# Kernel optimization log

Hardware: AMD Instinct MI355X
Metric: run time of the kernel (lower is better)

## Reference

```python
import jax, jax.numpy as jnp
import numpy as np

B, T, DM, DS = 8, 2048, 1024, 256
BASE_DECAY = 0.05


def _lin(k, out_dim, in_dim):
    return jax.random.normal(k, (out_dim, in_dim), jnp.float32) / np.sqrt(in_dim).astype(np.float32)


def setup_inputs() -> dict:
    key = jax.random.key(0)
    ks = jax.random.split(key, 18)
    return {
        "x": jax.random.normal(ks[0], (B, T, DM), jnp.float32),
        "prev_state": jax.random.normal(ks[1], (B, DS), jnp.float32),
        "W_in": _lin(ks[2], DS, DM),
        "W_x": _lin(ks[3], DS, DM),
        "W_s": _lin(ks[4], DS, DS),
        "W_out": _lin(ks[5], DM, DS),
        "W_gx": _lin(ks[6], DS, DM),
        "b_gx": jax.random.normal(ks[7], (DS,), jnp.float32) * 0.02,
        "W_gs": _lin(ks[8], DS, DS),
        "b_gs": jax.random.normal(ks[9], (DS,), jnp.float32) * 0.02,
        "W_dc": _lin(ks[10], DS, DM + DS),
        "b_dc": jax.random.normal(ks[11], (DS,), jnp.float32) * 0.02,
        "W_pp": _lin(ks[12], DS, 2 * DS),
        "b_pp": jax.random.normal(ks[13], (DS,), jnp.float32) * 0.02,
        "W_pg": _lin(ks[14], DS, DS),
        "b_pg": jax.random.normal(ks[15], (DS,), jnp.float32) * 0.02,
    }


def reference(x, prev_state, W_in, W_x, W_s, W_out, W_gx, b_gx, W_gs, b_gs,
              W_dc, b_dc, W_pp, b_pp, W_pg, b_pg):
    # torch Linear: y = x @ W.T (+ b); W is [out, in]
    lin = lambda v, W: jnp.einsum('bti,oi->bto', v, W)
    Bx, Tx, _ = x.shape
    delta = lin(x, W_in)                                   # [B,T,DS]
    s_prev = jnp.broadcast_to(prev_state[:, None, :], (Bx, Tx, prev_state.shape[-1]))
    ctx = jnp.concatenate([x, s_prev], axis=-1)            # [B,T,DM+DS]
    decay = jnp.exp(-BASE_DECAY * jnp.clip(jax.nn.sigmoid(lin(ctx, W_dc) + b_dc), 0.0, 1.0))
    s_pred = s_prev * decay + delta + lin(x, W_x) + 0.5 * lin(s_prev, W_s)
    perturb_in = jnp.concatenate([s_pred, s_prev], axis=-1)  # [B,T,2*DS]
    perturb_vec = jnp.tanh(lin(perturb_in, W_pp) + b_pp)
    perturb_strength = jax.nn.sigmoid(lin(s_prev, W_pg) + b_pg)
    s_corrected = s_pred + perturb_strength * perturb_vec
    gate_in = jax.nn.sigmoid(lin(x, W_gx) + b_gx)
    gate_state = jax.nn.sigmoid(lin(s_prev, W_gs) + b_gs)
    h = s_corrected * gate_in * gate_state
    out = lin(h, W_out)                                    # [B,T,DM]
    return out, h[:, -1, :]
```

## Files before the change

kernel.cpp:

```cpp
#include <hip/hip_runtime.h>
#include <hip/hip_bf16.h>
#include <math.h>


typedef __attribute__((ext_vector_type(4)))  float f32x4;
typedef __attribute__((ext_vector_type(8)))  short bf16x8;

#define DEV static __device__ __forceinline__

DEV float bf2f(short u) {
  union { float f; unsigned i; } v; v.i = ((unsigned)(unsigned short)u) << 16; return v.f;
}
DEV short f2bf(float f) {
  union { float f; unsigned i; } v; v.f = f;
  unsigned x = v.i;
  return (short)((x + 0x7fffu + ((x >> 16) & 1u)) >> 16);
}
DEV unsigned pk_bf16(float lo, float hi) {
  __hip_bfloat162 h = __float22bfloat162_rn(make_float2(lo, hi));
  return *(unsigned*)&h;
}
DEV float sigmoidf_(float x) { return 1.f / (1.f + expf(-x)); }

DEV void gl16(const void* g, void* l) {
  __builtin_amdgcn_global_load_lds(
      (const __attribute__((address_space(1))) void*)(g),
      (__attribute__((address_space(3))) void*)(l), 16, 0, 0);
}

static const size_t OFF_Y    = 0;
static const size_t OFF_XBF  = 25165824;
static const size_t OFF_S    = OFF_XBF;
static const size_t OFF_G    = OFF_XBF + 8388608;
static const size_t OFF_WCAT = OFF_XBF + 33554432;
static const size_t OFF_WPP  = OFF_WCAT + 1572864;
static const size_t OFF_WOUT = OFF_WPP + 131072;
static const size_t OFF_VEC  = OFF_WOUT + 524288;

__global__ __launch_bounds__(256, 1) void prep_all_k(
    const float* __restrict__ x, short* __restrict__ xbf,
    const float* __restrict__ W_in, const float* __restrict__ W_x,
    const float* __restrict__ W_gx, const float* __restrict__ W_dc,
    const float* __restrict__ W_pp, const float* __restrict__ W_out,
    short* __restrict__ wcat, short* __restrict__ wpp, short* __restrict__ wout,
    const float* __restrict__ prev, const float* __restrict__ Ws,
    const float* __restrict__ bdc, const float* __restrict__ bpp,
    const float* __restrict__ Wpg, const float* __restrict__ bpg,
    const float* __restrict__ Wgs, const float* __restrict__ bgs,
    float* __restrict__ vecs) {
  const int bid = (int)blockIdx.x, tid = (int)threadIdx.x;
  if (bid < 8192) {
    const size_t i = ((size_t)bid * 256 + tid) * 8;
    const float4 a = *(const float4*)(x + i);
    const float4 b = *(const float4*)(x + i + 4);
    uint4 o;
    o.x = pk_bf16(a.x, a.y); o.y = pk_bf16(a.z, a.w);
    o.z = pk_bf16(b.x, b.y); o.w = pk_bf16(b.z, b.w);
    *(uint4*)(xbf + i) = o;
  } else if (bid < 12544) {
    const int idx = (bid - 8192) * 256 + tid;
    const int N_WCAT = 768 * 1024, N_WPP = 256 * 256;
    if (idx < N_WCAT) {
      const int r = idx >> 10, k = idx & 1023;
      float v;
      if (r < 256)      v = W_in[r * 1024 + k] + W_x[r * 1024 + k];
      else if (r < 512) v = W_gx[(r - 256) * 1024 + k];
      else              v = W_dc[(r - 512) * 1280 + k];
      wcat[idx] = f2bf(v);
    } else if (idx < N_WCAT + N_WPP) {
      const int j = idx - N_WCAT, o = j >> 8, k = j & 255;
      wpp[j] = f2bf(W_pp[o * 512 + k]);
    } else {
      const int j = idx - N_WCAT - N_WPP, o = j >> 8, k = j & 255;
      wout[j] = f2bf(W_out[o * 256 + k]);
    }
  } else {
    const int sb = bid - 12544;
    const int b = sb / 20, rem = sb % 20, m = rem >> 2, oq = rem & 3;
    const int lane = tid & 63, w = tid >> 6;
    const float4 sv = *(const float4*)(prev + b * 256 + lane * 4);
    const float* Wb; const float* bias; int stride, off;
    if (m == 0)      { Wb = W_dc; stride = 1280; off = 1024; bias = bdc; }
    else if (m == 1) { Wb = Ws;   stride = 256;  off = 0;    bias = nullptr; }
    else if (m == 2) { Wb = W_pp; stride = 512;  off = 256;  bias = bpp; }
    else if (m == 3) { Wb = Wpg;  stride = 256;  off = 0;    bias = bpg; }
    else             { Wb = Wgs;  stride = 256;  off = 0;    bias = bgs; }
    const int o0 = oq * 64 + w * 16;
#pragma unroll 4
    for (int i = 0; i < 16; ++i) {
      const int o = o0 + i;
      const float4 wv = *(const float4*)(Wb + (size_t)o * stride + off + lane * 4);
      float p = wv.x * sv.x + wv.y * sv.y + wv.z * sv.z + wv.w * sv.w;
#pragma unroll
      for (int d = 32; d >= 1; d >>= 1) p += __shfl_xor(p, d, 64);
      if (lane == 0) {
        float r = (m == 1) ? 0.5f * p : p + bias[o];
        if (m >= 3) r = sigmoidf_(r);
        vecs[m * 2048 + b * 256 + o] = r;
      }
    }
  }
}

__global__ __launch_bounds__(512, 2) void gemm1_8p_k(const short* __restrict__ A,
                                                     const short* __restrict__ Bm,
                                                     short* __restrict__ Y) {
  __shared__ short As[4][8192];
  __shared__ short Bs[4][8192];
  const int tid = (int)threadIdx.x, lane = tid & 63, w = tid >> 6;
  const int wm = w >> 2, wn = w & 3;
  int bid = (int)blockIdx.x;
  bid = (bid & 7) * 24 + (bid >> 3);
  const int mt = bid / 3, nt = bid % 3;
  const int m0 = mt * 256;
  const short* gA = A + (size_t)m0 * 1024;
  const short* gB = Bm + (size_t)(nt * 256) * 1024;

  f32x4 acc[8][4];
#pragma unroll
  for (int mi = 0; mi < 8; ++mi)
#pragma unroll
    for (int ni = 0; ni < 4; ++ni)
#pragma unroll
      for (int r = 0; r < 4; ++r) acc[mi][ni][r] = 0.f;

#define STG(gax, lds, half, t)                                                \
  {                                                                           \
    _Pragma("unroll")                                                         \
    for (int j = 0; j < 2; ++j) {                                             \
      const int G = j * 512 + tid, r = G >> 3, g = G & 7;                     \
      gl16(gax + (size_t)((half) * 128 + r) * 1024 + (t) * 64 +               \
               ((g ^ (r & 7)) * 8),                                           \
           (lds) + G * 8);                                                    \
    }                                                                         \
  }

  STG(gA, As[0], 0, 0); STG(gA, As[1], 1, 0);
  STG(gB, Bs[0], 0, 0); STG(gB, Bs[1], 1, 0);
  STG(gA, As[2], 0, 1);
  asm volatile("s_waitcnt vmcnt(2)" ::: "memory");
  __builtin_amdgcn_s_barrier();

  const int arow = lane & 15, ag = lane >> 4;
  bf16x8 af[4][2], bfv[2][2];
#pragma unroll 1
  for (int t = 0; t < 16; ++t) {
    const short* sA = As[(2 * t + wm) & 3];
    const short* sB = Bs[(2 * t + (wn >> 1)) & 3];
#pragma unroll
    for (int q = 0; q < 4; ++q) {
      const int qm = q >> 1, qn = q & 1;
      if (qn == 0) {
#pragma unroll
        for (int fi = 0; fi < 4; ++fi) {
          const int r = qm * 64 + fi * 16 + arow;
#pragma unroll
          for (int ks = 0; ks < 2; ++ks)
            af[fi][ks] = *(const bf16x8*)(sA + r * 64 + (((ks * 4 + ag) ^ (r & 7)) << 3));
        }
      }
#pragma unroll
      for (int fj = 0; fj < 2; ++fj) {
        const int r = (wn & 1) * 64 + qn * 32 + fj * 16 + arow;
#pragma unroll
        for (int ks = 0; ks < 2; ++ks)
          bfv[fj][ks] = *(const bf16x8*)(sB + r * 64 + (((ks * 4 + ag) ^ (r & 7)) << 3));
      }
      if (q == 0) {
        if (t + 1 < 16) {
          STG(gB, Bs[(2 * t + 2) & 3], 0, t + 1);
          STG(gA, As[(2 * t + 3) & 3], 1, t + 1);
          STG(gB, Bs[(2 * t + 3) & 3], 1, t + 1);
        }
      } else if (q == 3) {
        if (t + 2 < 16) STG(gA, As[(2 * t + 4) & 3], 0, t + 2);
        if (t <= 13)      { asm volatile("s_waitcnt vmcnt(2)" ::: "memory"); }
        else if (t == 14) { asm volatile("s_waitcnt vmcnt(0)" ::: "memory"); }
      }
      __builtin_amdgcn_s_barrier();
      asm volatile("s_waitcnt lgkmcnt(0)" ::: "memory");
      __builtin_amdgcn_sched_barrier(0);
      __builtin_amdgcn_s_setprio(1);
#pragma unroll
      for (int fi = 0; fi < 4; ++fi)
#pragma unroll
        for (int fj = 0; fj < 2; ++fj)
#pragma unroll
          for (int ks = 0; ks < 2; ++ks)
            acc[qm * 4 + fi][qn * 2 + fj] = __builtin_amdgcn_mfma_f32_16x16x32_bf16(
                af[fi][ks], bfv[fj][ks], acc[qm * 4 + fi][qn * 2 + fj], 0, 0, 0);
      __builtin_amdgcn_s_setprio(0);
      __builtin_amdgcn_s_barrier();
    }
  }
#undef STG

#pragma unroll
  for (int mi = 0; mi < 8; ++mi)
#pragma unroll
    for (int ni = 0; ni < 4; ++ni) {
      const int col = nt * 256 + wn * 64 + ni * 16 + (lane & 15);
#pragma unroll
      for (int r = 0; r < 4; ++r) {
        const int row = m0 + wm * 128 + mi * 16 + (lane >> 4) * 4 + r;
        Y[(size_t)row * 768 + col] = f2bf(acc[mi][ni][r]);
      }
    }
}

__global__ __launch_bounds__(256, 1) void elem1_k(const short* __restrict__ Y,
                                                  const float* __restrict__ prev,
                                                  const float* __restrict__ bgx,
                                                  const float* __restrict__ vecs,
                                                  short* __restrict__ S,
                                                  short* __restrict__ G) {
  const int t = (int)blockIdx.x * 256 + (int)threadIdx.x;
  const int row = t >> 5, gi = t & 31, j0 = gi * 8;
  const int b = row >> 11;
  const short* yr = Y + (size_t)row * 768;
  const bf16x8 yix = *(const bf16x8*)(yr + j0);
  const bf16x8 ygx = *(const bf16x8*)(yr + 256 + j0);
  const bf16x8 ydc = *(const bf16x8*)(yr + 512 + j0);
  bf16x8 so, go;
#pragma unroll
  for (int j = 0; j < 8; ++j) {
    const int c = b * 256 + j0 + j;
    const float dcl = bf2f(ydc[j]) + vecs[0 * 2048 + c];
    const float dec = expf(-0.05f * sigmoidf_(dcl));
    const float sp = prev[c] * dec + bf2f(yix[j]) + vecs[1 * 2048 + c];
    const float g = sigmoidf_(bf2f(ygx[j]) + bgx[j0 + j]);
    so[j] = f2bf(sp); go[j] = f2bf(g);
  }
  *(bf16x8*)(S + (size_t)row * 256 + j0) = so;
  *(bf16x8*)(G + (size_t)row * 256 + j0) = go;
}

__global__ __launch_bounds__(256) void gemm2h_k(const short* __restrict__ S,
                                                const short* __restrict__ G,
                                                const short* __restrict__ Wpp,
                                                const float* __restrict__ vecs,
                                                short* __restrict__ H,
                                                float* __restrict__ out) {
  __shared__ short As2[2][2048];
  __shared__ short Bs2[2][4096];
  const int tid = (int)threadIdx.x, lane = tid & 63, w = tid >> 6;
  const int wr = w >> 1, wc = w & 1;
  int bid = (int)blockIdx.x;
  bid = (bid & 7) * 64 + (bid >> 3);
  const int m0 = (bid >> 1) * 64, n0 = (bid & 1) * 128;
  const int b = m0 >> 11;
  const short* gA = S + (size_t)m0 * 256;
  const short* gB = Wpp + (size_t)n0 * 256;

  f32x4 acc[2][4];
#pragma unroll
  for (int mi = 0; mi < 2; ++mi)
#pragma unroll
    for (int ni = 0; ni < 4; ++ni)
#pragma unroll
      for (int r = 0; r < 4; ++r) acc[mi][ni][r] = 0.f;

#define STAGE2(buf, t)                                                        \
  {                                                                           \
    {                                                                         \
      const int g = tid;                                                      \
      gl16(gA + (size_t)(g >> 2) * 256 + (t) * 32 + (g & 3) * 8,              \
           As2[buf] + w * 512);                                               \
    }                                                                         \
    _Pragma("unroll")                                                         \
    for (int j = 0; j < 2; ++j) {                                             \
      const int g = j * 256 + tid;                                            \
      gl16(gB + (size_t)(g >> 2) * 256 + (t) * 32 + (g & 3) * 8,              \
           Bs2[buf] + (j * 256 + w * 64) * 8);                                \
    }                                                                         \
  }

  STAGE2(0, 0);
  __syncthreads();
  const int arow = lane & 15, ag = lane >> 4;
#pragma unroll 1
  for (int t = 0; t < 8; ++t) {
    if (t < 7) STAGE2((t + 1) & 1, t + 1);
    const short* Asb = As2[t & 1];
    const short* Bsb = Bs2[t & 1];
    bf16x8 af[2], bfv[4];
#pragma unroll
    for (int mi = 0; mi < 2; ++mi)
      af[mi] = *(const bf16x8*)(Asb + (wr * 32 + mi * 16 + arow) * 32 + ag * 8);
#pragma unroll
    for (int ni = 0; ni < 4; ++ni)
      bfv[ni] = *(const bf16x8*)(Bsb + (wc * 64 + ni * 16 + arow) * 32 + ag * 8);
#pragma unroll
    for (int mi = 0; mi < 2; ++mi)
#pragma unroll
      for (int ni = 0; ni < 4; ++ni)
        acc[mi][ni] = __builtin_amdgcn_mfma_f32_16x16x32_bf16(af[mi], bfv[ni], acc[mi][ni], 0, 0, 0);
    __syncthreads();
  }
#undef STAGE2

#pragma unroll
  for (int mi = 0; mi < 2; ++mi)
#pragma unroll
    for (int ni = 0; ni < 4; ++ni) {
      const int col = n0 + wc * 64 + ni * 16 + (lane & 15);
      const float spp  = vecs[2 * 2048 + b * 256 + col];
      const float pstr = vecs[3 * 2048 + b * 256 + col];
      const float gst  = vecs[4 * 2048 + b * 256 + col];
#pragma unroll
      for (int r = 0; r < 4; ++r) {
        const int row = m0 + wr * 32 + mi * 16 + (lane >> 4) * 4 + r;
        const float pv = tanhf(acc[mi][ni][r] + spp);
        const float sp = bf2f(S[(size_t)row * 256 + col]);
        const float h = (sp + pstr * pv) * bf2f(G[(size_t)row * 256 + col]) * gst;
        H[(size_t)row * 256 + col] = f2bf(h);
        if ((row & 2047) == 2047) out[16777216 + b * 256 + col] = h;
      }
    }
}

__global__ __launch_bounds__(256) void gemm3_k(const short* __restrict__ H,
                                               const short* __restrict__ Wout,
                                               float* __restrict__ out) {
  __shared__ short As3[2][2048];
  __shared__ short Bs3[2][8192];
  const int tid = (int)threadIdx.x, lane = tid & 63, w = tid >> 6;
  const int wr = w >> 1, wc = w & 1;
  int bid = (int)blockIdx.x;
  bid = (bid & 7) * 128 + (bid >> 3);
  const int m0 = (bid >> 2) * 64, n0 = (bid & 3) * 256;
  const short* gA = H + (size_t)m0 * 256;
  const short* gB = Wout + (size_t)n0 * 256;

  f32x4 acc[2][8];
#pragma unroll
  for (int mi = 0; mi < 2; ++mi)
#pragma unroll
    for (int ni = 0; ni < 8; ++ni)
#pragma unroll
      for (int r = 0; r < 4; ++r) acc[mi][ni][r] = 0.f;

#define STAGE3(buf, t)                                                        \
  {                                                                           \
    {                                                                         \
      const int g = tid;                                                      \
      gl16(gA + (size_t)(g >> 2) * 256 + (t) * 32 + (g & 3) * 8,              \
           As3[buf] + w * 512);                                               \
    }                                                                         \
    _Pragma("unroll")                                                         \
    for (int j = 0; j < 4; ++j) {                                             \
      const int g = j * 256 + tid;                                            \
      gl16(gB + (size_t)(g >> 2) * 256 + (t) * 32 + (g & 3) * 8,              \
           Bs3[buf] + (j * 256 + w * 64) * 8);                                \
    }                                                                         \
  }

  STAGE3(0, 0);
  __syncthreads();
  const int arow = lane & 15, ag = lane >> 4;
#pragma unroll 1
  for (int t = 0; t < 8; ++t) {
    if (t < 7) STAGE3((t + 1) & 1, t + 1);
    const short* Asb = As3[t & 1];
    const short* Bsb = Bs3[t & 1];
    bf16x8 af[2], bfv[8];
#pragma unroll
    for (int mi = 0; mi < 2; ++mi)
      af[mi] = *(const bf16x8*)(Asb + (wr * 32 + mi * 16 + arow) * 32 + ag * 8);
#pragma unroll
    for (int ni = 0; ni < 8; ++ni)
      bfv[ni] = *(const bf16x8*)(Bsb + (wc * 128 + ni * 16 + arow) * 32 + ag * 8);
#pragma unroll
    for (int mi = 0; mi < 2; ++mi)
#pragma unroll
      for (int ni = 0; ni < 8; ++ni)
        acc[mi][ni] = __builtin_amdgcn_mfma_f32_16x16x32_bf16(af[mi], bfv[ni], acc[mi][ni], 0, 0, 0);
    __syncthreads();
  }
#undef STAGE3

#pragma unroll
  for (int mi = 0; mi < 2; ++mi)
#pragma unroll
    for (int ni = 0; ni < 8; ++ni) {
      const int col = n0 + wc * 128 + ni * 16 + (lane & 15);
#pragma unroll
      for (int r = 0; r < 4; ++r) {
        const int row = m0 + wr * 32 + mi * 16 + (lane >> 4) * 4 + r;
        out[(size_t)row * 1024 + col] = acc[mi][ni][r];
      }
    }
}

extern "C" void kernel_launch(void* const* d_in, const int* in_sizes, int n_in,
                              void* d_out, int out_size, void* d_ws, size_t ws_size,
                              hipStream_t stream) {
  (void)in_sizes; (void)n_in; (void)out_size; (void)ws_size;
  const float* x      = (const float*)d_in[0];
  const float* prev   = (const float*)d_in[1];
  const float* W_in   = (const float*)d_in[2];
  const float* W_x    = (const float*)d_in[3];
  const float* W_s    = (const float*)d_in[4];
  const float* W_out  = (const float*)d_in[5];
  const float* W_gx   = (const float*)d_in[6];
  const float* b_gx   = (const float*)d_in[7];
  const float* W_gs   = (const float*)d_in[8];
  const float* b_gs   = (const float*)d_in[9];
  const float* W_dc   = (const float*)d_in[10];
  const float* b_dc   = (const float*)d_in[11];
  const float* W_pp   = (const float*)d_in[12];
  const float* b_pp   = (const float*)d_in[13];
  const float* W_pg   = (const float*)d_in[14];
  const float* b_pg   = (const float*)d_in[15];

  char* ws = (char*)d_ws;
  short* Y    = (short*)(ws + OFF_Y);
  short* H    = (short*)(ws + OFF_Y);
  short* xbf  = (short*)(ws + OFF_XBF);
  short* S    = (short*)(ws + OFF_S);
  short* G    = (short*)(ws + OFF_G);
  short* wcat = (short*)(ws + OFF_WCAT);
  short* wpp  = (short*)(ws + OFF_WPP);
  short* wout = (short*)(ws + OFF_WOUT);
  float* vecs = (float*)(ws + OFF_VEC);
  float* out  = (float*)d_out;

  prep_all_k<<<12704, 256, 0, stream>>>(x, xbf, W_in, W_x, W_gx, W_dc, W_pp, W_out,
                                        wcat, wpp, wout, prev, W_s, b_dc, b_pp,
                                        W_pg, b_pg, W_gs, b_gs, vecs);
  gemm1_8p_k<<<192, 512, 0, stream>>>(xbf, wcat, Y);
  elem1_k<<<2048, 256, 0, stream>>>(Y, prev, b_gx, vecs, S, G);
  gemm2h_k<<<512, 256, 0, stream>>>(S, G, wpp, vecs, H, out);
  gemm3_k<<<1024, 256, 0, stream>>>(H, wout, out);
}
```

Baseline: 117.9 us.

## Fuse elementwise state/gate epilogue into first GEMM via interleaved weight layout

Reorders the concatenated first-GEMM weight so each 192-row group holds the matching 64 columns of the combined in/x, gate, and decay projections. Each block can then compute S and G directly in its epilogue, which removes the Y intermediate write/read and the separate elem1 launch. The GEMM tiling changes from 256x256 tiles with 8x4 accumulators to 256x192 tiles with 2x12 per wave over 256 blocks. The B stage now uses 2 buffers instead of 4. The epilogue writes scattered bf16 stores rather than vectors, and H now aliases the xbf region.

```diff
diff --git a/kernel.cpp b/kernel.cpp
--- a/kernel.cpp
+++ b/kernel.cpp
@@ -28,10 +28,9 @@
       (__attribute__((address_space(3))) void*)(l), 16, 0, 0);
 }
 
-static const size_t OFF_Y    = 0;
+static const size_t OFF_S    = 0;
+static const size_t OFF_G    = 8388608;
 static const size_t OFF_XBF  = 25165824;
-static const size_t OFF_S    = OFF_XBF;
-static const size_t OFF_G    = OFF_XBF + 8388608;
 static const size_t OFF_WCAT = OFF_XBF + 33554432;
 static const size_t OFF_WPP  = OFF_WCAT + 1572864;
 static const size_t OFF_WOUT = OFF_WPP + 131072;
@@ -62,10 +61,11 @@
     const int N_WCAT = 768 * 1024, N_WPP = 256 * 256;
     if (idx < N_WCAT) {
       const int r = idx >> 10, k = idx & 1023;
+      const int g = r / 192, j = r % 192;
       float v;
-      if (r < 256)      v = W_in[r * 1024 + k] + W_x[r * 1024 + k];
-      else if (r < 512) v = W_gx[(r - 256) * 1024 + k];
-      else              v = W_dc[(r - 512) * 1280 + k];
+      if (j < 64)       v = W_in[(g * 64 + j) * 1024 + k] + W_x[(g * 64 + j) * 1024 + k];
+      else if (j < 128) v = W_gx[(g * 64 + j - 64) * 1024 + k];
+      else              v = W_dc[(g * 64 + j - 128) * 1280 + k];
       wcat[idx] = f2bf(v);
     } else if (idx < N_WCAT + N_WPP) {
       const int j = idx - N_WCAT, o = j >> 8, k = j & 255;
@@ -102,137 +102,132 @@
   }
 }
 
-__global__ __launch_bounds__(512, 2) void gemm1_8p_k(const short* __restrict__ A,
-                                                     const short* __restrict__ Bm,
-                                                     short* __restrict__ Y) {
+__global__ __launch_bounds__(512) void gemm1sg8p_k(const short* __restrict__ A,
+                                                   const short* __restrict__ Bm,
+                                                   const float* __restrict__ prev,
+                                                   const float* __restrict__ bgx,
+                                                   const float* __restrict__ vecs,
+                                                   short* __restrict__ S,
+                                                   short* __restrict__ G) {
   __shared__ short As[4][8192];
-  __shared__ short Bs[4][8192];
+  __shared__ short Bs[2][12288];
   const int tid = (int)threadIdx.x, lane = tid & 63, w = tid >> 6;
-  const int wm = w >> 2, wn = w & 3;
   int bid = (int)blockIdx.x;
-  bid = (bid & 7) * 24 + (bid >> 3);
-  const int mt = bid / 3, nt = bid % 3;
-  const int m0 = mt * 256;
+  bid = (bid & 7) * 32 + (bid >> 3);
+  const int mt = bid >> 2, grp = bid & 3;
+  const int m0 = mt * 256, b = m0 >> 11;
   const short* gA = A + (size_t)m0 * 1024;
-  const short* gB = Bm + (size_t)(nt * 256) * 1024;
-
-  f32x4 acc[8][4];
-#pragma unroll
-  for (int mi = 0; mi < 8; ++mi)
-#pragma unroll
-    for (int ni = 0; ni < 4; ++ni)
+  const short* gB = Bm + (size_t)(grp * 192) * 1024;
+
+  f32x4 acc[2][12];
+#pragma unroll
+  for (int mi = 0; mi < 2; ++mi)
+#pragma unroll
+    for (int ni = 0; ni < 12; ++ni)
 #pragma unroll
       for (int r = 0; r < 4; ++r) acc[mi][ni][r] = 0.f;
 
-#define STG(gax, lds, half, t)                                                \
+#define STGA(lds, half, t)                                                    \
   {                                                                           \
     _Pragma("unroll")                                                         \
     for (int j = 0; j < 2; ++j) {                                             \
-      const int G = j * 512 + tid, r = G >> 3, g = G & 7;                     \
-      gl16(gax + (size_t)((half) * 128 + r) * 1024 + (t) * 64 +               \
+      const int Gr = j * 512 + tid, r = Gr >> 3, g = Gr & 7;                  \
+      gl16(gA + (size_t)((half) * 128 + r) * 1024 + (t) * 64 +                \
                ((g ^ (r & 7)) * 8),                                           \
-           (lds) + G * 8);                                                    \
-    }                                                                         \
-  }
-
-  STG(gA, As[0], 0, 0); STG(gA, As[1], 1, 0);
-  STG(gB, Bs[0], 0, 0); STG(gB, Bs[1], 1, 0);
-  STG(gA, As[2], 0, 1);
+           (lds) + Gr * 8);                                                   \
+    }                                                                         \
+  }
+#define STGB(lds, t)                                                          \
+  {                                                                           \
+    _Pragma("unroll")                                                         \
+    for (int j = 0; j < 3; ++j) {                                             \
+      const int Gr = j * 512 + tid, r = Gr >> 3, g = Gr & 7;                  \
+      gl16(gB + (size_t)r * 1024 + (t) * 64 + ((g ^ (r & 7)) * 8),            \
+           (lds) + Gr * 8);                                                   \
+    }                                                                         \
+  }
+
+  STGA(As[0], 0, 0); STGA(As[1], 1, 0);
+  STGB(Bs[0], 0);
+  STGA(As[2], 0, 1);
   asm volatile("s_waitcnt vmcnt(2)" ::: "memory");
   __builtin_amdgcn_s_barrier();
 
   const int arow = lane & 15, ag = lane >> 4;
-  bf16x8 af[4][2], bfv[2][2];
+  const int rA = (w & 3) * 32;
+  const int hA = w >> 2;
+  bf16x8 af[2][2], bfv[4][2];
 #pragma unroll 1
   for (int t = 0; t < 16; ++t) {
-    const short* sA = As[(2 * t + wm) & 3];
-    const short* sB = Bs[(2 * t + (wn >> 1)) & 3];
-#pragma unroll
-    for (int q = 0; q < 4; ++q) {
-      const int qm = q >> 1, qn = q & 1;
-      if (qn == 0) {
-#pragma unroll
-        for (int fi = 0; fi < 4; ++fi) {
-          const int r = qm * 64 + fi * 16 + arow;
+    const short* sA = As[(2 * t + hA) & 3];
+    const short* sB = Bs[t & 1];
+#pragma unroll
+    for (int q = 0; q < 3; ++q) {
+      if (q == 0) {
+#pragma unroll
+        for (int mi = 0; mi < 2; ++mi) {
+          const int r = rA + mi * 16 + arow;
 #pragma unroll
           for (int ks = 0; ks < 2; ++ks)
-            af[fi][ks] = *(const bf16x8*)(sA + r * 64 + (((ks * 4 + ag) ^ (r & 7)) << 3));
+            af[mi][ks] = *(const bf16x8*)(sA + r * 64 + (((ks * 4 + ag) ^ (r & 7)) << 3));
         }
       }
 #pragma unroll
-      for (int fj = 0; fj < 2; ++fj) {
-        const int r = (wn & 1) * 64 + qn * 32 + fj * 16 + arow;
+      for (int fj = 0; fj < 4; ++fj) {
+        const int r = q * 64 + fj * 16 + arow;
 #pragma unroll
         for (int ks = 0; ks < 2; ++ks)
           bfv[fj][ks] = *(const bf16x8*)(sB + r * 64 + (((ks * 4 + ag) ^ (r & 7)) << 3));
       }
       if (q == 0) {
         if (t + 1 < 16) {
-          STG(gB, Bs[(2 * t + 2) & 3], 0, t + 1);
-          STG(gA, As[(2 * t + 3) & 3], 1, t + 1);
-          STG(gB, Bs[(2 * t + 3) & 3], 1, t + 1);
+          STGB(Bs[(t + 1) & 1], t + 1);
+          STGA(As[(2 * t + 3) & 3], 1, t + 1);
         }
-      } else if (q == 3) {
-        if (t + 2 < 16) STG(gA, As[(2 * t + 4) & 3], 0, t + 2);
-        if (t <= 13)      { asm volatile("s_waitcnt vmcnt(2)" ::: "memory"); }
-        else if (t == 14) { asm volatile("s_waitcnt vmcnt(0)" ::: "memory"); }
+      } else if (q == 2) {
+        if (t + 2 < 16) STGA(As[(2 * t + 4) & 3], 0, t + 2);
+        if (t <= 13) { asm volatile("s_waitcnt vmcnt(2)" ::: "memory"); }
+        else         { asm volatile("s_waitcnt vmcnt(0)" ::: "memory"); }
       }
       __builtin_amdgcn_s_barrier();
       asm volatile("s_waitcnt lgkmcnt(0)" ::: "memory");
       __builtin_amdgcn_sched_barrier(0);
       __builtin_amdgcn_s_setprio(1);
 #pragma unroll
-      for (int fi = 0; fi < 4; ++fi)
-#pragma unroll
-        for (int fj = 0; fj < 2; ++fj)
+      for (int mi = 0; mi < 2; ++mi)
+#pragma unroll
+        for (int fj = 0; fj < 4; ++fj)
 #pragma unroll
           for (int ks = 0; ks < 2; ++ks)
-            acc[qm * 4 + fi][qn * 2 + fj] = __builtin_amdgcn_mfma_f32_16x16x32_bf16(
-                af[fi][ks], bfv[fj][ks], acc[qm * 4 + fi][qn * 2 + fj], 0, 0, 0);
+            acc[mi][q * 4 + fj] = __builtin_amdgcn_mfma_f32_16x16x32_bf16(
+                af[mi][ks], bfv[fj][ks], acc[mi][q * 4 + fj], 0, 0, 0);
       __builtin_amdgcn_s_setprio(0);
       __builtin_amdgcn_s_barrier();
     }
   }
-#undef STG
-
-#pragma unroll
-  for (int mi = 0; mi < 8; ++mi)
-#pragma unroll
-    for (int ni = 0; ni < 4; ++ni) {
-      const int col = nt * 256 + wn * 64 + ni * 16 + (lane & 15);
+#undef STGA
+#undef STGB
+
+  const int quad = lane >> 4;
+#pragma unroll
+  for (int cidx = 0; cidx < 4; ++cidx) {
+    const int cg = grp * 64 + cidx * 16 + arow;
+    const float sdc = vecs[0 * 2048 + b * 256 + cg];
+    const float sws = vecs[1 * 2048 + b * 256 + cg];
+    const float pv  = prev[b * 256 + cg];
+    const float bg  = bgx[cg];
+#pragma unroll
+    for (int mi = 0; mi < 2; ++mi)
 #pragma unroll
       for (int r = 0; r < 4; ++r) {
-        const int row = m0 + wm * 128 + mi * 16 + (lane >> 4) * 4 + r;
-        Y[(size_t)row * 768 + col] = f2bf(acc[mi][ni][r]);
-      }
-    }
-}
-
-__global__ __launch_bounds__(256, 1) void elem1_k(const short* __restrict__ Y,
-                                                  const float* __restrict__ prev,
-                                                  const float* __restrict__ bgx,
-                                                  const float* __restrict__ vecs,
-                                                  short* __restrict__ S,
-                                                  short* __restrict__ G) {
-  const int t = (int)blockIdx.x * 256 + (int)threadIdx.x;
-  const int row = t >> 5, gi = t & 31, j0 = gi * 8;
-  const int b = row >> 11;
-  const short* yr = Y + (size_t)row * 768;
-  const bf16x8 yix = *(const bf16x8*)(yr + j0);
-  const bf16x8 ygx = *(const bf16x8*)(yr + 256 + j0);
-  const bf16x8 ydc = *(const bf16x8*)(yr + 512 + j0);
-  bf16x8 so, go;
-#pragma unroll
-  for (int j = 0; j < 8; ++j) {
-    const int c = b * 256 + j0 + j;
-    const float dcl = bf2f(ydc[j]) + vecs[0 * 2048 + c];
-    const float dec = expf(-0.05f * sigmoidf_(dcl));
-    const float sp = prev[c] * dec + bf2f(yix[j]) + vecs[1 * 2048 + c];
-    const float g = sigmoidf_(bf2f(ygx[j]) + bgx[j0 + j]);
-    so[j] = f2bf(sp); go[j] = f2bf(g);
-  }
-  *(bf16x8*)(S + (size_t)row * 256 + j0) = so;
-  *(bf16x8*)(G + (size_t)row * 256 + j0) = go;
+        const int row = m0 + w * 32 + mi * 16 + quad * 4 + r;
+        const float dec = expf(-0.05f * sigmoidf_(acc[mi][8 + cidx][r] + sdc));
+        const float sp = pv * dec + acc[mi][cidx][r] + sws;
+        const float g = sigmoidf_(acc[mi][4 + cidx][r] + bg);
+        S[(size_t)row * 256 + cg] = f2bf(sp);
+        G[(size_t)row * 256 + cg] = f2bf(g);
+      }
+  }
 }
 
 __global__ __launch_bounds__(256) void gemm2h_k(const short* __restrict__ S,
@@ -414,11 +409,10 @@
   const float* b_pg   = (const float*)d_in[15];
 
   char* ws = (char*)d_ws;
-  short* Y    = (short*)(ws + OFF_Y);
-  short* H    = (short*)(ws + OFF_Y);
-  short* xbf  = (short*)(ws + OFF_XBF);
   short* S    = (short*)(ws + OFF_S);
   short* G    = (short*)(ws + OFF_G);
+  short* xbf  = (short*)(ws + OFF_XBF);
+  short* H    = (short*)(ws + OFF_XBF);
   short* wcat = (short*)(ws + OFF_WCAT);
   short* wpp  = (short*)(ws + OFF_WPP);
   short* wout = (short*)(ws + OFF_WOUT);
@@ -428,8 +422,7 @@
   prep_all_k<<<12704, 256, 0, stream>>>(x, xbf, W_in, W_x, W_gx, W_dc, W_pp, W_out,
                                         wcat, wpp, wout, prev, W_s, b_dc, b_pp,
                                         W_pg, b_pg, W_gs, b_gs, vecs);
-  gemm1_8p_k<<<192, 512, 0, stream>>>(xbf, wcat, Y);
-  elem1_k<<<2048, 256, 0, stream>>>(Y, prev, b_gx, vecs, S, G);
+  gemm1sg8p_k<<<256, 512, 0, stream>>>(xbf, wcat, prev, b_gx, vecs, S, G);
   gemm2h_k<<<512, 256, 0, stream>>>(S, G, wpp, vecs, H, out);
   gemm3_k<<<1024, 256, 0, stream>>>(H, wout, out);
 }
```

After: 103.1 us. -12.5%, faster.
